# Kernel optimization log

Hardware: AMD Instinct MI355X
Metric: run time of the kernel (lower is better)

The kernel has to match this reference:

```python
import jax, jax.numpy as jnp
import numpy as np

N_NODES = 30000
N_EDGES = 300000
C = 16          # multiplicity of input scalars and of each output irrep
SH_SPLITS = [(0, 1), (1, 4), (4, 9)]  # l=0,1,2 slices of edge_sh


def setup_inputs() -> dict:
    key = jax.random.key(0)
    ks = jax.random.split(key, 7)
    node_feat = jax.random.normal(ks[0], (N_NODES, C), dtype=jnp.float32)
    edge_index = jax.random.randint(ks[1], (2, N_EDGES), 0, N_NODES, dtype=jnp.int64)
    edge_sh = jax.random.normal(ks[2], (N_EDGES, 9), dtype=jnp.float32)
    edge_radial = jax.random.uniform(ks[3], (N_EDGES, 16), dtype=jnp.float32)
    W1 = jax.random.normal(ks[4], (16, 64), dtype=jnp.float32)     # radial net layer 1
    W2 = jax.random.normal(ks[5], (64, 3 * C * C), dtype=jnp.float32)  # -> tp.weight_numel = 768
    W_si = jax.random.normal(ks[6], (C, C), dtype=jnp.float32)     # self-interaction 0e->0e
    return {"node_feat": node_feat, "edge_index": edge_index, "edge_sh": edge_sh,
            "edge_radial": edge_radial, "W1": W1, "W2": W2, "W_si": W_si}


def reference(node_feat, edge_index, edge_sh, edge_radial, W1, W2, W_si):
    N, c = node_feat.shape  # c == C
    src, dst = edge_index[0], edge_index[1]

    # Radial MLP (e3nn FullyConnectedNet style: weight / sqrt(fan_in), silu, no bias)
    h = jax.nn.silu(edge_radial @ (W1 / jnp.sqrt(jnp.asarray(W1.shape[0], W1.dtype))))
    tpw = h @ (W2 / jnp.sqrt(jnp.asarray(W2.shape[0], W2.dtype)))  # (E, 768)
    tpw = tpw.reshape(-1, 3, c, c)  # (E, l, u, v)

    # Gather source scalars and mix multiplicities per path (0e x l -> l, CG = identity)
    x = node_feat[src]                                   # (E, C)
    mix = jnp.einsum('eu,eluv->elv', x, tpw) / jnp.sqrt(jnp.asarray(c, x.dtype))  # (E,3,C)

    # Outer product with each SH degree; e3nn mul-major layout (v, m)
    msgs = []
    for l, (a, b) in enumerate(SH_SPLITS):
        m = mix[:, l, :, None] * edge_sh[:, None, a:b]   # (E, C, 2l+1)
        msgs.append(m.reshape(m.shape[0], -1))
    messages = jnp.concatenate(msgs, axis=-1)            # (E, 144)

    # Scatter-add to destination nodes
    agg = jax.ops.segment_sum(messages, dst, num_segments=N)  # (N, 144)

    # Self-interaction: equivariant Linear, only 0e->0e path; l>0 outputs are zero
    si_scalar = node_feat @ (W_si / jnp.sqrt(jnp.asarray(c, node_feat.dtype)))  # (N, C)
    si = jnp.concatenate([si_scalar, jnp.zeros((N, 8 * c), si_scalar.dtype)], axis=-1)
    return agg + si
```

## Files before the change

### kernel.cpp

```cpp
#include <hip/hip_runtime.h>


typedef _Float16 f16x2 __attribute__((ext_vector_type(2)));
typedef _Float16 f16x8 __attribute__((ext_vector_type(8)));
typedef __fp16  g16x2 __attribute__((ext_vector_type(2)));
typedef float f32x4 __attribute__((ext_vector_type(4)));

union AFrag { unsigned int u[4]; f16x2 h2[4]; f16x8 v; };
union BFrag { uint4 u4; f16x8 v; };
union HW { g16x2 g; f16x2 f; unsigned int u; };


__global__ __launch_bounds__(256)
void prep_kernel(const float* __restrict__ W2, const float* __restrict__ W1,
                 _Float16* __restrict__ bfrag, _Float16* __restrict__ w1frag,
                 const int* __restrict__ ei, int* __restrict__ counts, int E) {
    int t = blockIdx.x * 256 + threadIdx.x;
    if (t < E) atomicAdd(&counts[ei[E + t] + 1], 1);
    if (t < 96 * 512) {
        int f = t >> 9;
        int rr = t & 511;
        int lane = rr >> 3, j = rr & 7;
        int ks = f / 3, nt = f - 3 * ks;
        int q = lane >> 4, c = lane & 15;
        int ku = ks * 32 + q * 8 + j;
        int k = ku >> 4, u = ku & 15;
        int n = nt * 16 + c;
        int l = n >> 4, v = n & 15;
        float val = W2[(size_t)k * 768 + l * 256 + u * 16 + v] * 0.03125f;
        bfrag[t] = (_Float16)val;
    }
    if (t < 2048) {
        int nt = t >> 9, rr = t & 511;
        int lane = rr >> 3, j = rr & 7;
        int q = lane >> 4, c = lane & 15;
        int u = q * 8 + j;
        float val = (q < 2) ? W1[u * 64 + nt * 16 + c] * 0.25f : 0.0f;
        w1frag[t] = (_Float16)val;
    }
}

__global__ __launch_bounds__(1024)
void scan_kernel(int* __restrict__ data, int n_pad) {
    __shared__ int wsum[16];
    __shared__ int carry_s;
    int tid = threadIdx.x, lane = tid & 63, wid = tid >> 6;
    if (tid == 0) carry_s = 0;
    __syncthreads();
    for (int base = 0; base < n_pad; base += 32768) {
        int beg = base + tid * 32;
        int4 c0[8];
        #pragma unroll
        for (int j = 0; j < 8; ++j)
            c0[j] = *(const int4*)(data + beg + j * 4);
        int s = 0;
        #pragma unroll
        for (int j = 0; j < 8; ++j) s += c0[j].x + c0[j].y + c0[j].z + c0[j].w;

        int v = s;
        #pragma unroll
        for (int off = 1; off < 64; off <<= 1) {
            int t = __shfl_up(v, off, 64);
            if (lane >= off) v += t;
        }
        if (lane == 63) wsum[wid] = v;
        __syncthreads();
        if (wid == 0 && lane < 16) {
            int w = wsum[lane];
            #pragma unroll
            for (int off = 1; off < 16; off <<= 1) {
                int t = __shfl_up(w, off, 16);
                if (lane >= off) w += t;
            }
            wsum[lane] = w;
        }
        __syncthreads();
        int run = carry_s + (v - s) + (wid > 0 ? wsum[wid - 1] : 0);
        #pragma unroll
        for (int j = 0; j < 8; ++j) {
            int4 o;
            run += c0[j].x; o.x = run;
            run += c0[j].y; o.y = run;
            run += c0[j].z; o.z = run;
            run += c0[j].w; o.w = run;
            *(int4*)(data + beg + j * 4) = o;
        }
        __syncthreads();
        if (tid == 1023) carry_s = run;
        __syncthreads();
    }
}


__global__ __launch_bounds__(64, 4)
void edge_mfma_kernel(const float* __restrict__ nf, const int* __restrict__ ei,
                      const float* __restrict__ radial,
                      const _Float16* __restrict__ w1frag,
                      const float* __restrict__ sh,
                      const _Float16* __restrict__ bfrag,
                      const int* __restrict__ offs, int* __restrict__ curs,
                      unsigned int* __restrict__ rows, int E) {
    __shared__ unsigned int h_lds[64][32];

    int lane = threadIdx.x & 63;
    int r_ = lane & 15;
    int q  = lane >> 4;
    int qh = q >> 1;
    int ul = (q & 1) * 8;
    unsigned int sel = qh ? 0x03020302u : 0x01000100u;

    int ebase = blockIdx.x * 64;

    HW xp[4][4];
    #pragma unroll
    for (int m = 0; m < 4; ++m) {
        int e = ebase + m * 16 + r_; if (e >= E) e = E - 1;
        int src = ei[e];
        const float* xpp = nf + (size_t)src * 16 + ul;
        float4 a = *(const float4*)xpp;
        float4 b = *(const float4*)(xpp + 4);
        xp[m][0].g = __builtin_amdgcn_cvt_pkrtz(a.x, a.y);
        xp[m][1].g = __builtin_amdgcn_cvt_pkrtz(a.z, a.w);
        xp[m][2].g = __builtin_amdgcn_cvt_pkrtz(b.x, b.y);
        xp[m][3].g = __builtin_amdgcn_cvt_pkrtz(b.z, b.w);
    }

    int p = 0;
    {
        int e = ebase + lane;
        if (e < E) {
            int dst = ei[E + e];
            p = offs[dst] + atomicAdd(&curs[dst], 1);
            const float* s = sh + (size_t)e * 9;
            float4 s03 = *(const float4*)s;
            float4 s47 = *(const float4*)(s + 4);
            float s8 = s[8];
            unsigned int* d = rows + (size_t)p * 32 + 24;
            HW w0, w1, w2, w3, w4;
            w0.g = __builtin_amdgcn_cvt_pkrtz(s03.x, s03.y);
            w1.g = __builtin_amdgcn_cvt_pkrtz(s03.z, s03.w);
            w2.g = __builtin_amdgcn_cvt_pkrtz(s47.x, s47.y);
            w3.g = __builtin_amdgcn_cvt_pkrtz(s47.z, s47.w);
            w4.g = __builtin_amdgcn_cvt_pkrtz(s8, 0.0f);
            d[0] = w0.u; d[1] = w1.u; d[2] = w2.u; d[3] = w3.u; d[4] = w4.u;
        }
    }

    {
        BFrag wf[4];
        #pragma unroll
        for (int nt = 0; nt < 4; ++nt)
            wf[nt].u4 = *(const uint4*)(w1frag + (size_t)nt * 512 + lane * 8);

        #pragma unroll
        for (int m = 0; m < 4; ++m) {
            AFrag ra;
            if (q < 2) {
                int e = ebase + m * 16 + r_; if (e >= E) e = E - 1;
                const float* rp = radial + (size_t)e * 16 + q * 8;
                float4 a = *(const float4*)rp;
                float4 b = *(const float4*)(rp + 4);
                HW t0, t1, t2, t3;
                t0.g = __builtin_amdgcn_cvt_pkrtz(a.x, a.y);
                t1.g = __builtin_amdgcn_cvt_pkrtz(a.z, a.w);
                t2.g = __builtin_amdgcn_cvt_pkrtz(b.x, b.y);
                t3.g = __builtin_amdgcn_cvt_pkrtz(b.z, b.w);
                ra.u[0] = t0.u; ra.u[1] = t1.u; ra.u[2] = t2.u; ra.u[3] = t3.u;
            } else {
                ra.u[0] = 0; ra.u[1] = 0; ra.u[2] = 0; ra.u[3] = 0;
            }
            #pragma unroll
            for (int nt = 0; nt < 4; ++nt) {
                f32x4 z4 = __builtin_amdgcn_mfma_f32_16x16x32_f16(
                    ra.v, wf[nt].v, (f32x4){0.f, 0.f, 0.f, 0.f}, 0, 0, 0);
                #pragma unroll
                for (int i = 0; i < 4; ++i) {
                    float z = z4[i];
                    float h = z * __builtin_amdgcn_rcpf(1.0f + __expf(-z));
                    float hn = __shfl_xor(h, 1);
                    if (!(r_ & 1)) {
                        int el = m * 16 + q * 4 + i;
                        HW w; w.g = __builtin_amdgcn_cvt_pkrtz(h, hn);
                        h_lds[el][((nt << 3) + (r_ >> 1)) ^ (el & 31)] = w.u;
                    }
                }
            }
        }
    }

    f32x4 acc[4][3];
    #pragma unroll
    for (int m = 0; m < 4; ++m)
        #pragma unroll
        for (int nt = 0; nt < 3; ++nt)
            acc[m][nt] = (f32x4){0.f, 0.f, 0.f, 0.f};

    auto compute = [&](int ks, BFrag (&b)[3]) {
        #pragma unroll
        for (int m = 0; m < 4; ++m) {
            int el = m * 16 + r_;
            unsigned int hw = h_lds[el][ks ^ (el & 31)];
            HW hv; hv.u = __builtin_amdgcn_perm(hw, hw, sel);
            AFrag a;
            #pragma unroll
            for (int p2 = 0; p2 < 4; ++p2)
                a.h2[p2] = hv.f * xp[m][p2].f;
            #pragma unroll
            for (int nt = 0; nt < 3; ++nt)
                acc[m][nt] = __builtin_amdgcn_mfma_f32_16x16x32_f16(a.v, b[nt].v, acc[m][nt], 0, 0, 0);
        }
    };

    BFrag bA[3], bB[3];
    #pragma unroll
    for (int nt = 0; nt < 3; ++nt)
        bA[nt].u4 = *(const uint4*)(bfrag + (size_t)nt * 512 + lane * 8);
    for (int ks = 0; ks < 32; ks += 2) {
        #pragma unroll
        for (int nt = 0; nt < 3; ++nt)
            bB[nt].u4 = *(const uint4*)(bfrag + (size_t)((ks + 1) * 3 + nt) * 512 + lane * 8);
        compute(ks, bA);
        #pragma unroll
        for (int nt = 0; nt < 3; ++nt)
            bA[nt].u4 = *(const uint4*)(bfrag + (size_t)((ks + 2) * 3 + nt) * 512 + lane * 8);
        compute(ks + 1, bB);
    }

    _Float16* rowh = (_Float16*)rows;
    #pragma unroll
    for (int m = 0; m < 4; ++m) {
        #pragma unroll
        for (int i = 0; i < 4; ++i) {
            int el = m * 16 + q * 4 + i;
            int e = ebase + el;
            int pe = __shfl(p, el, 64);
            if (e < E) {
                HW pr; pr.g = __builtin_amdgcn_cvt_pkrtz(acc[m][0][i], acc[m][1][i]);
                rows[(size_t)pe * 32 + r_] = pr.u;
                rowh[(size_t)pe * 64 + 32 + r_] = (_Float16)acc[m][2][i];
            }
        }
    }
}


__global__ __launch_bounds__(256)
void gather_kernel(const unsigned int* __restrict__ rows,
                   const int* __restrict__ offs,
                   const float* __restrict__ nf, const float* __restrict__ Wsi,
                   float* __restrict__ out, int N) {
    int node = blockIdx.x * 4 + (threadIdx.x >> 6);
    if (node >= N) return;
    int lane = threadIdx.x & 63;
    int half = (lane >= 24 && lane < 48) ? 1 : 0;
    int w = lane - half * 24;
    bool active = lane < 48;
    bool isP = active && (w < 16);
    bool isQ = active && (w >= 16) && (w < 24);
    int t = w - 16;

    HW accP0, accP1; accP0.u = 0; accP1.u = 0;
    HW accQ0, accQ1, accQ2, accQ3, accQ4, accQ5;
    accQ0.u = accQ1.u = accQ2.u = accQ3.u = accQ4.u = accQ5.u = 0;

    int off = offs[node], end = offs[node + 1];
    int i = off;

    auto do_pair = [&](int ibase, bool pred) {
        int idx = ibase + half;
        bool valid = !pred || (idx < end);
        int ic = valid ? idx : ibase;
        const unsigned int* rb = rows + (size_t)ic * 32;
        unsigned int M = 0, Sa = 0, Sb = 0, Sc = 0;
        if (active) M = rb[w];
        if (isP) { Sa = rb[24]; Sb = rb[25]; }
        if (isQ) { Sa = rb[26]; Sb = rb[27]; Sc = rb[28]; }
        if (!valid) { Sa = 0; Sb = 0; Sc = 0; }
        HW m_, sa, sb, sc; m_.u = M; sa.u = Sa; sb.u = Sb; sc.u = Sc;
        if (isP) {
            accP0.f += m_.f * sa.f;
            HW mh; mh.u = __builtin_amdgcn_perm(M, M, 0x03020302u);
            accP1.f += mh.f * sb.f;
        }
        if (isQ) {
            HW ma; ma.u = __builtin_amdgcn_perm(M, M, 0x01000100u);
            HW mb; mb.u = __builtin_amdgcn_perm(M, M, 0x03020302u);
            accQ0.f += ma.f * sa.f;
            accQ1.f += ma.f * sb.f;
            accQ2.f += ma.f * sc.f;
            accQ3.f += mb.f * sa.f;
            accQ4.f += mb.f * sb.f;
            accQ5.f += mb.f * sc.f;
        }
    };

    for (; i + 7 < end; i += 8) {
        #pragma unroll
        for (int jp = 0; jp < 4; ++jp) do_pair(i + 2 * jp, false);
    }
    for (; i < end; i += 2) do_pair(i, true);

    {
        int o;
        o = __shfl((int)accP0.u, lane + 24, 64); if (lane < 24) { HW h_; h_.u = (unsigned)o; accP0.f += h_.f; }
        o = __shfl((int)accP1.u, lane + 24, 64); if (lane < 24) { HW h_; h_.u = (unsigned)o; accP1.f += h_.f; }
        o = __shfl((int)accQ0.u, lane + 24, 64); if (lane < 24) { HW h_; h_.u = (unsigned)o; accQ0.f += h_.f; }
        o = __shfl((int)accQ1.u, lane + 24, 64); if (lane < 24) { HW h_; h_.u = (unsigned)o; accQ1.f += h_.f; }
        o = __shfl((int)accQ2.u, lane + 24, 64); if (lane < 24) { HW h_; h_.u = (unsigned)o; accQ2.f += h_.f; }
        o = __shfl((int)accQ3.u, lane + 24, 64); if (lane < 24) { HW h_; h_.u = (unsigned)o; accQ3.f += h_.f; }
        o = __shfl((int)accQ4.u, lane + 24, 64); if (lane < 24) { HW h_; h_.u = (unsigned)o; accQ4.f += h_.f; }
        o = __shfl((int)accQ5.u, lane + 24, 64); if (lane < 24) { HW h_; h_.u = (unsigned)o; accQ5.f += h_.f; }
    }

    if (lane >= 24) return;
    float* orow = out + (size_t)node * 144;
    if (w < 16) {
        float c0 = (float)accP0.f[0];
        float c1 = (float)accP0.f[1];
        float c2 = (float)accP1.f[0];
        float c3 = (float)accP1.f[1];
        const float* xr = nf + (size_t)node * 16;
        float si = 0.0f;
        #pragma unroll
        for (int u = 0; u < 16; ++u)
            si = fmaf(xr[u], Wsi[u * 16 + w], si);
        c0 = fmaf(si, 0.25f, c0);
        orow[w] = c0;
        orow[16 + 3 * w + 0] = c1;
        orow[16 + 3 * w + 1] = c2;
        orow[16 + 3 * w + 2] = c3;
    } else {
        float* qp = orow + 64 + 10 * t;
        qp[0] = (float)accQ0.f[0]; qp[1] = (float)accQ0.f[1];
        qp[2] = (float)accQ1.f[0]; qp[3] = (float)accQ1.f[1];
        qp[4] = (float)accQ2.f[0];
        qp[5] = (float)accQ3.f[0]; qp[6] = (float)accQ3.f[1];
        qp[7] = (float)accQ4.f[0]; qp[8] = (float)accQ4.f[1];
        qp[9] = (float)accQ5.f[0];
    }
}


__global__ __launch_bounds__(256)
void si_init_kernel(const float* __restrict__ nf, const float* __restrict__ Wsi,
                    float* __restrict__ out, int N) {
    int t = blockIdx.x * blockDim.x + threadIdx.x;
    int total = N * 144;
    if (t >= total) return;
    int n = t / 144;
    int c = t - n * 144;
    float val = 0.0f;
    if (c < 16) {
        const float* xr = nf + n * 16;
        #pragma unroll
        for (int u = 0; u < 16; ++u)
            val = fmaf(xr[u], Wsi[u * 16 + c], val);
        val *= 0.25f;
    }
    out[t] = val;
}

__global__ __launch_bounds__(256)
void edge_kernel_atomic(const float* __restrict__ nf, const int* __restrict__ ei,
                        const float* __restrict__ sh, const float* __restrict__ radial,
                        const float* __restrict__ W1, const float* __restrict__ W2,
                        float* __restrict__ out, int E) {
    int e = blockIdx.x * blockDim.x + threadIdx.x;
    if (e >= E) return;
    int src = ei[e];
    int dst = ei[E + e];
    float r[16], x[16];
    #pragma unroll
    for (int u = 0; u < 16; ++u) r[u] = radial[e * 16 + u] * 0.25f;
    #pragma unroll
    for (int u = 0; u < 16; ++u) x[u] = nf[src * 16 + u] * 0.03125f;
    float acc[48];
    #pragma unroll
    for (int j = 0; j < 48; ++j) acc[j] = 0.0f;
    for (int k = 0; k < 64; ++k) {
        float z = 0.0f;
        #pragma unroll
        for (int u = 0; u < 16; ++u) z = fmaf(r[u], W1[u * 64 + k], z);
        float hk = z / (1.0f + __expf(-z));
        const float* w2k = W2 + k * 768;
        #pragma unroll 4
        for (int u = 0; u < 16; ++u) {
            float p = hk * x[u];
            const float* w = w2k + u * 16;
            #pragma unroll
            for (int l = 0; l < 3; ++l)
                #pragma unroll
                for (int v = 0; v < 16; ++v)
                    acc[l * 16 + v] = fmaf(p, w[l * 256 + v], acc[l * 16 + v]);
        }
    }
    const float* she = sh + e * 9;
    float* orow = out + (long)dst * 144;
    #pragma unroll
    for (int v = 0; v < 16; ++v) atomicAdd(&orow[v], acc[v] * she[0]);
    #pragma unroll
    for (int v = 0; v < 16; ++v)
        for (int m = 0; m < 3; ++m)
            atomicAdd(&orow[16 + v * 3 + m], acc[16 + v] * she[1 + m]);
    #pragma unroll
    for (int v = 0; v < 16; ++v)
        for (int m = 0; m < 5; ++m)
            atomicAdd(&orow[64 + v * 5 + m], acc[32 + v] * she[4 + m]);
}


extern "C" void kernel_launch(void* const* d_in, const int* in_sizes, int n_in,
                              void* d_out, int out_size, void* d_ws, size_t ws_size,
                              hipStream_t stream) {
    const float* nf     = (const float*)d_in[0];
    const int*   ei     = (const int*)  d_in[1];
    const float* sh     = (const float*)d_in[2];
    const float* radial = (const float*)d_in[3];
    const float* W1     = (const float*)d_in[4];
    const float* W2     = (const float*)d_in[5];
    const float* Wsi    = (const float*)d_in[6];
    float* out = (float*)d_out;

    const int N = in_sizes[0] / 16;
    const int E = in_sizes[1] / 2;

    int n_scan = N + 1;
    int n_pad  = (n_scan + 32767) & ~32767;

    size_t rows_bytes = (size_t)E * 128;
    size_t offs_bytes = (size_t)n_pad * sizeof(int);
    size_t curs_bytes = (size_t)N * sizeof(int);
    size_t bfrag_off  = (rows_bytes + offs_bytes + curs_bytes + 127) & ~(size_t)127;
    size_t bfrag_bytes = 102 * 512 * sizeof(_Float16);
    size_t w1f_off    = bfrag_off + bfrag_bytes;
    size_t w1f_bytes  = 2048 * sizeof(_Float16);
    size_t need = w1f_off + w1f_bytes;

    if (ws_size < need) {
        int total = N * 144;
        hipLaunchKernelGGL(si_init_kernel, dim3((total + 255) / 256), dim3(256), 0, stream,
                           nf, Wsi, out, N);
        hipLaunchKernelGGL(edge_kernel_atomic, dim3((E + 255) / 256), dim3(256), 0, stream,
                           nf, ei, sh, radial, W1, W2, out, E);
        return;
    }

    char* wsb = (char*)d_ws;
    unsigned int* rows = (unsigned int*)wsb;
    int*   offs = (int*)(wsb + rows_bytes);
    int*   curs = (int*)(wsb + rows_bytes + offs_bytes);
    _Float16* bfrag = (_Float16*)(wsb + bfrag_off);
    _Float16* w1frag = (_Float16*)(wsb + w1f_off);

    (void)hipMemsetAsync(offs, 0, offs_bytes + curs_bytes, stream);

    int eb256 = (E + 255) / 256;
    hipLaunchKernelGGL(prep_kernel, dim3(eb256), dim3(256), 0, stream,
                       W2, W1, bfrag, w1frag, ei, offs, E);
    hipLaunchKernelGGL(scan_kernel, dim3(1), dim3(1024), 0, stream, offs, n_pad);
    int eb64 = (E + 63) / 64;
    hipLaunchKernelGGL(edge_mfma_kernel, dim3(eb64), dim3(64), 0, stream,
                       nf, ei, radial, w1frag, sh, bfrag, offs, curs, rows, E);
    hipLaunchKernelGGL(gather_kernel, dim3((N + 3) / 4), dim3(256), 0, stream,
                       rows, offs, nf, Wsi, out, N);
}
```

Measured before the change: 109.5 us.

## Write edge rows in edge order and gather via a sorted edge-index permutation

Edge rows are no longer written at their destination-sorted slot. The edge kernel writes them contiguously by edge id, and a new scatter kernel builds a permutation array of edge ids sorted by destination. The gather kernel reads each row through that permutation. This turns the scattered writes into coalesced ones and moves the atomic out of the MFMA kernel, at the cost of an extra launch, an extra indirection and random 128-byte row reads in the gather.

After: 128.6 us. 1.17x slower.

```diff
diff --git a/kernel.cpp b/kernel.cpp
--- a/kernel.cpp
+++ b/kernel.cpp
@@ -91,6 +91,16 @@
     }
 }
 
+__global__ __launch_bounds__(256)
+void scatter_kernel(const int* __restrict__ ei, const int* __restrict__ offs,
+                    int* __restrict__ cursor, int* __restrict__ eord, int E) {
+    int e = blockIdx.x * blockDim.x + threadIdx.x;
+    if (e >= E) return;
+    int dst = ei[E + e];
+    int p = offs[dst] + atomicAdd(&cursor[dst], 1);
+    eord[p] = e;
+}
+
 
 __global__ __launch_bounds__(64, 4)
 void edge_mfma_kernel(const float* __restrict__ nf, const int* __restrict__ ei,
@@ -98,7 +108,6 @@
                       const _Float16* __restrict__ w1frag,
                       const float* __restrict__ sh,
                       const _Float16* __restrict__ bfrag,
-                      const int* __restrict__ offs, int* __restrict__ curs,
                       unsigned int* __restrict__ rows, int E) {
     __shared__ unsigned int h_lds[64][32];
 
@@ -125,17 +134,14 @@
         xp[m][3].g = __builtin_amdgcn_cvt_pkrtz(b.z, b.w);
     }
 
-    int p = 0;
     {
         int e = ebase + lane;
         if (e < E) {
-            int dst = ei[E + e];
-            p = offs[dst] + atomicAdd(&curs[dst], 1);
             const float* s = sh + (size_t)e * 9;
             float4 s03 = *(const float4*)s;
             float4 s47 = *(const float4*)(s + 4);
             float s8 = s[8];
-            unsigned int* d = rows + (size_t)p * 32 + 24;
+            unsigned int* d = rows + (size_t)e * 32 + 24;
             HW w0, w1, w2, w3, w4;
             w0.g = __builtin_amdgcn_cvt_pkrtz(s03.x, s03.y);
             w1.g = __builtin_amdgcn_cvt_pkrtz(s03.z, s03.w);
@@ -233,11 +239,10 @@
         for (int i = 0; i < 4; ++i) {
             int el = m * 16 + q * 4 + i;
             int e = ebase + el;
-            int pe = __shfl(p, el, 64);
             if (e < E) {
                 HW pr; pr.g = __builtin_amdgcn_cvt_pkrtz(acc[m][0][i], acc[m][1][i]);
-                rows[(size_t)pe * 32 + r_] = pr.u;
-                rowh[(size_t)pe * 64 + 32 + r_] = (_Float16)acc[m][2][i];
+                rows[(size_t)e * 32 + r_] = pr.u;
+                rowh[(size_t)e * 64 + 32 + r_] = (_Float16)acc[m][2][i];
             }
         }
     }
@@ -246,6 +251,7 @@
 
 __global__ __launch_bounds__(256)
 void gather_kernel(const unsigned int* __restrict__ rows,
+                   const int* __restrict__ eord,
                    const int* __restrict__ offs,
                    const float* __restrict__ nf, const float* __restrict__ Wsi,
                    float* __restrict__ out, int N) {
@@ -270,7 +276,8 @@
         int idx = ibase + half;
         bool valid = !pred || (idx < end);
         int ic = valid ? idx : ibase;
-        const unsigned int* rb = rows + (size_t)ic * 32;
+        int er = eord[ic];
+        const unsigned int* rb = rows + (size_t)er * 32;
         unsigned int M = 0, Sa = 0, Sb = 0, Sc = 0;
         if (active) M = rb[w];
         if (isP) { Sa = rb[24]; Sb = rb[25]; }
@@ -430,7 +437,8 @@
     size_t rows_bytes = (size_t)E * 128;
     size_t offs_bytes = (size_t)n_pad * sizeof(int);
     size_t curs_bytes = (size_t)N * sizeof(int);
-    size_t bfrag_off  = (rows_bytes + offs_bytes + curs_bytes + 127) & ~(size_t)127;
+    size_t eord_bytes = (size_t)E * sizeof(int);
+    size_t bfrag_off  = (rows_bytes + offs_bytes + curs_bytes + eord_bytes + 127) & ~(size_t)127;
     size_t bfrag_bytes = 102 * 512 * sizeof(_Float16);
     size_t w1f_off    = bfrag_off + bfrag_bytes;
     size_t w1f_bytes  = 2048 * sizeof(_Float16);
@@ -449,6 +457,7 @@
     unsigned int* rows = (unsigned int*)wsb;
     int*   offs = (int*)(wsb + rows_bytes);
     int*   curs = (int*)(wsb + rows_bytes + offs_bytes);
+    int*   eord = (int*)(wsb + rows_bytes + offs_bytes + curs_bytes);
     _Float16* bfrag = (_Float16*)(wsb + bfrag_off);
     _Float16* w1frag = (_Float16*)(wsb + w1f_off);
 
@@ -458,9 +467,11 @@
     hipLaunchKernelGGL(prep_kernel, dim3(eb256), dim3(256), 0, stream,
                        W2, W1, bfrag, w1frag, ei, offs, E);
     hipLaunchKernelGGL(scan_kernel, dim3(1), dim3(1024), 0, stream, offs, n_pad);
+    hipLaunchKernelGGL(scatter_kernel, dim3(eb256), dim3(256), 0, stream,
+                       ei, offs, curs, eord, E);
     int eb64 = (E + 63) / 64;
     hipLaunchKernelGGL(edge_mfma_kernel, dim3(eb64), dim3(64), 0, stream,
-                       nf, ei, radial, w1frag, sh, bfrag, offs, curs, rows, E);
+                       nf, ei, radial, w1frag, sh, bfrag, rows, E);
     hipLaunchKernelGGL(gather_kernel, dim3((N + 3) / 4), dim3(256), 0, stream,
-                       rows, offs, nf, Wsi, out, N);
-}
+                       rows, eord, offs, nf, Wsi, out, N);
+}
```
